# Kernel optimization log

Hardware: AMD Instinct MI355X
Metric: run time of the kernel (lower is better)

The kernel has to match this reference:

```python
import jax, jax.numpy as jnp
import numpy as np

NTOKEN = 150000   # len(ui2idx)
NINP   = 64       # opt.d_word_vec
NHID   = 2 * NINP # gnn1 output dim
NEDGE  = 2400000  # hetero static graph edges
B, L   = 64, 200  # batch_size, max_len


def setup_inputs() -> dict:
    key = jax.random.key(0)
    ks = jax.random.split(key, 8)
    def xavier(k, shape):
        scale = (2.0 / (shape[0] + shape[1])) ** 0.5
        return scale * jax.random.normal(k, shape, jnp.float32)
    emb = xavier(ks[0], (NTOKEN, NINP)).at[0].set(0.0)  # padding_idx=0
    W1 = xavier(ks[1], (NINP, NHID))
    b1 = jnp.zeros((NHID,), jnp.float32)
    W2 = xavier(ks[2], (NHID, NINP))
    b2 = jnp.zeros((NINP,), jnp.float32)
    edge_index = jax.random.randint(ks[3], (2, NEDGE), 0, NTOKEN, dtype=jnp.int32).astype(jnp.int64)
    inp = jax.random.randint(ks[4], (B, L), 0, NTOKEN, dtype=jnp.int32).astype(jnp.int64)
    input_timestamp = jax.random.randint(ks[5], (B, L), 0, 300000, dtype=jnp.int32).astype(jnp.int64)
    return {"emb": emb, "W1": W1, "b1": b1, "W2": W2, "b2": b2,
            "input": inp, "input_timestamp": input_timestamp, "edge_index": edge_index}


def gcn_conv(x, W, b, src, dst, n):
    # torch_geometric GCNConv: out = D^{-1/2}(A+I)D^{-1/2} (x W) + b
    h = x @ W                                   # [n, out]
    deg = jnp.zeros((n,), h.dtype).at[dst].add(1.0) + 1.0  # +1 self-loop
    dinv = jax.lax.rsqrt(deg)
    norm = dinv[src] * dinv[dst]                # [E]
    agg = jax.ops.segment_sum(h[src] * norm[:, None], dst, num_segments=n)
    return agg + h * (dinv * dinv)[:, None] + b  # self-loop term + bias


def reference(emb, W1, b1, W2, b2, input, input_timestamp, edge_index):
    src, dst = edge_index[0], edge_index[1]
    h = gcn_conv(emb, W1, b1, src, dst, NTOKEN)      # dropout is identity in eval
    nodes = gcn_conv(h, W2, b2, src, dst, NTOKEN)    # [NTOKEN, NINP]
    # one-hot scatter + einsum 'bt,td->bd' == direct gather
    b_, l_ = input.shape
    return nodes[input.reshape(-1)].reshape(b_, l_, NINP)
```

## Files before the change

kernel.cpp:

```cpp
#include <hip/hip_runtime.h>
#include <hip/hip_bf16.h>

#define NTOKEN 150000
#define NINP   64
#define NEDGE  2400000
#define NPOS   (64*200)

#define NPB    256
#define NBUCK  586
#define EPB    4096
#define NBLK   586
#define CAPS   4480

#define NXB    1172

#define O_XBF      0
#define O_Z1       4800000
#define O_BUCK     9600000
#define O_GCUR     12225280
#define O_DINV     12225920
#define O_RS       12375936
#define O_M        12525952
#define O_CVEC     12530048

__device__ __forceinline__ unsigned f2bf(float f) {
    unsigned u = __float_as_uint(f);
    return (u + 0x7FFFu + ((u >> 16) & 1u)) >> 16;
}

__global__ void __launch_bounds__(1024) k1(
        const float4* __restrict__ X4, uint4* __restrict__ Xbf,
        const float* __restrict__ W1, const float* __restrict__ b1,
        const float* __restrict__ W2, float* __restrict__ M,
        float* __restrict__ cvec, int* __restrict__ gcur) {
    int t = threadIdx.x, B = blockIdx.x;
    if (B < NXB) {
        int i = B * 1024 + t;
        if (i < NTOKEN * 64 / 8) {
            float4 a = X4[2 * i], b = X4[2 * i + 1];
            uint4 o;
            o.x = f2bf(a.x) | (f2bf(a.y) << 16);
            o.y = f2bf(a.z) | (f2bf(a.w) << 16);
            o.z = f2bf(b.x) | (f2bf(b.y) << 16);
            o.w = f2bf(b.z) | (f2bf(b.w) << 16);
            Xbf[i] = o;
        }
    } else if (B < NXB + 4) {
        int o = (B - NXB) * 1024 + t;
        int i = o >> 6, j = o & 63;
        float s = 0.f;
        #pragma unroll 4
        for (int k = 0; k < 128; k++) s = fmaf(W1[i * 128 + k], W2[k * 64 + j], s);
        M[o] = s;
    } else if (B == NXB + 4) {
        if (t < 64) {
            float s = 0.f;
            #pragma unroll 4
            for (int k = 0; k < 128; k++) s = fmaf(b1[k], W2[k * 64 + t], s);
            cvec[t] = s;
        }
    } else {
        if (t < NBUCK) gcur[t] = t * CAPS;
    }
}

__global__ void __launch_bounds__(512) kC(
        const int4* __restrict__ src4, const int4* __restrict__ dst4,
        int* __restrict__ gcur, int* __restrict__ bucketPacked) {
    __shared__ int eS[EPB];
    __shared__ int eD[EPB];
    __shared__ int h[NBUCK];
    int t = threadIdx.x, B = blockIdx.x;
    for (int i = t; i < NBUCK; i += 512) h[i] = 0;
    __syncthreads();
    int base4 = B * (EPB / 4);
    int n4 = NEDGE / 4 - base4; if (n4 > EPB / 4) n4 = EPB / 4;
    for (int i = t; i < n4; i += 512) {
        int4 s = src4[base4 + i];
        int4 d = dst4[base4 + i];
        eS[4*i+0] = s.x; eS[4*i+1] = s.y; eS[4*i+2] = s.z; eS[4*i+3] = s.w;
        eD[4*i+0] = d.x; eD[4*i+1] = d.y; eD[4*i+2] = d.z; eD[4*i+3] = d.w;
        atomicAdd(&h[d.x >> 8], 1);
        atomicAdd(&h[d.y >> 8], 1);
        atomicAdd(&h[d.z >> 8], 1);
        atomicAdd(&h[d.w >> 8], 1);
    }
    __syncthreads();
    for (int b = t; b < NBUCK; b += 512) {
        int c = h[b];
        if (c) h[b] = atomicAdd(&gcur[b], c);
    }
    __syncthreads();
    int n = n4 * 4;
    for (int i = t; i < n; i += 512) {
        int d = eD[i];
        int b = d >> 8;
        int pos = atomicAdd(&h[b], 1);
        bucketPacked[pos] = (eS[i] << 8) | (d & 255);
    }
}

__global__ void __launch_bounds__(512) kDS(
        const int* __restrict__ gcur,
        int* __restrict__ bucketPacked ,
        float* __restrict__ dinv, int* __restrict__ rowStart) {
    __shared__ int srt[CAPS];
    __shared__ int cnt[NPB];
    __shared__ int sd[NPB];
    int t = threadIdx.x, b = blockIdx.x;
    int e0 = b * CAPS;
    int nE = gcur[b] - e0;
    if (t < NPB) cnt[t] = 0;
    __syncthreads();
    for (int i = t; i < nE; i += 512) atomicAdd(&cnt[bucketPacked[e0 + i] & 255], 1);
    __syncthreads();
    int c = 0;
    if (t < NPB) { c = cnt[t]; sd[t] = c; }
    __syncthreads();
    for (int off = 1; off < 256; off <<= 1) {
        int x = 0;
        if (t < NPB && t >= off) x = sd[t - off];
        __syncthreads();
        if (t < NPB) sd[t] += x;
        __syncthreads();
    }
    if (t < NPB) {
        int excl = sd[t] - c;
        cnt[t] = excl;
        int node = b * NPB + t;
        if (node < NTOKEN) {
            dinv[node] = rsqrtf((float)c + 1.0f);
            rowStart[node] = (e0 + excl) | (c << 22);
        }
    }
    __syncthreads();
    for (int i = t; i < nE; i += 512) {
        int p = bucketPacked[e0 + i];
        int pos = atomicAdd(&cnt[p & 255], 1);
        srt[pos] = p >> 8;
    }
    __syncthreads();
    for (int i = t; i < nE; i += 512) bucketPacked[e0 + i] = srt[i];
}

__global__ void k_agg(const uint2* __restrict__ Xb, const float* __restrict__ dinv,
                      const int* __restrict__ rowStart, const int* __restrict__ sortedSrc,
                      uint2* __restrict__ Z1b) {
    int g = threadIdx.x >> 4;
    int fl = threadIdx.x & 15;
    int v = blockIdx.x * 16 + g;
    unsigned rs = (unsigned)rowStart[v];
    int e0 = rs & 0x3FFFFF;
    int e1 = e0 + (rs >> 22);
    float dv = dinv[v];
    uint2 xsw = Xb[(size_t)v * 16 + fl];
    float a0x=0.f,a0y=0.f,a0z=0.f,a0w=0.f, a1x=0.f,a1y=0.f,a1z=0.f,a1w=0.f;
    float a2x=0.f,a2y=0.f,a2z=0.f,a2w=0.f, a3x=0.f,a3y=0.f,a3z=0.f,a3w=0.f;
    for (int e = e0; e < e1; e += 8) {
        int m1=e+1<e1, m2=e+2<e1, m3=e+3<e1, m4=e+4<e1, m5=e+5<e1, m6=e+6<e1, m7=e+7<e1;
        int u0 = sortedSrc[e];
        int u1 = sortedSrc[m1 ? e+1 : e];
        int u2 = sortedSrc[m2 ? e+2 : e];
        int u3 = sortedSrc[m3 ? e+3 : e];
        int u4 = sortedSrc[m4 ? e+4 : e];
        int u5 = sortedSrc[m5 ? e+5 : e];
        int u6 = sortedSrc[m6 ? e+6 : e];
        int u7 = sortedSrc[m7 ? e+7 : e];
        float d0 = dinv[u0];
        float d1 = m1 ? dinv[u1] : 0.f;
        float d2 = m2 ? dinv[u2] : 0.f;
        float d3 = m3 ? dinv[u3] : 0.f;
        float d4 = m4 ? dinv[u4] : 0.f;
        float d5 = m5 ? dinv[u5] : 0.f;
        float d6 = m6 ? dinv[u6] : 0.f;
        float d7 = m7 ? dinv[u7] : 0.f;
        uint2 w0 = Xb[(size_t)u0 * 16 + fl];
        uint2 w1 = Xb[(size_t)u1 * 16 + fl];
        uint2 w2 = Xb[(size_t)u2 * 16 + fl];
        uint2 w3 = Xb[(size_t)u3 * 16 + fl];
        uint2 w4 = Xb[(size_t)u4 * 16 + fl];
        uint2 w5 = Xb[(size_t)u5 * 16 + fl];
        uint2 w6 = Xb[(size_t)u6 * 16 + fl];
        uint2 w7 = Xb[(size_t)u7 * 16 + fl];
        #define ACC(d,w,AX,AY,AZ,AW) \
            AX = fmaf(d, __uint_as_float((w).x << 16), AX); \
            AY = fmaf(d, __uint_as_float((w).x & 0xFFFF0000u), AY); \
            AZ = fmaf(d, __uint_as_float((w).y << 16), AZ); \
            AW = fmaf(d, __uint_as_float((w).y & 0xFFFF0000u), AW);
        ACC(d0,w0,a0x,a0y,a0z,a0w)
        ACC(d1,w1,a1x,a1y,a1z,a1w)
        ACC(d2,w2,a2x,a2y,a2z,a2w)
        ACC(d3,w3,a3x,a3y,a3z,a3w)
        ACC(d4,w4,a0x,a0y,a0z,a0w)
        ACC(d5,w5,a1x,a1y,a1z,a1w)
        ACC(d6,w6,a2x,a2y,a2z,a2w)
        ACC(d7,w7,a3x,a3y,a3z,a3w)
        #undef ACC
    }
    float ax = (a0x + a1x) + (a2x + a3x);
    float ay = (a0y + a1y) + (a2y + a3y);
    float az = (a0z + a1z) + (a2z + a3z);
    float aw = (a0w + a1w) + (a2w + a3w);
    float c = dv * dv;
    float ox = c * fmaf(dv, __uint_as_float(xsw.x << 16),         ax);
    float oy = c * fmaf(dv, __uint_as_float(xsw.x & 0xFFFF0000u), ay);
    float oz = c * fmaf(dv, __uint_as_float(xsw.y << 16),         az);
    float ow = c * fmaf(dv, __uint_as_float(xsw.y & 0xFFFF0000u), aw);
    uint2 o;
    o.x = f2bf(ox) | (f2bf(oy) << 16);
    o.y = f2bf(oz) | (f2bf(ow) << 16);
    Z1b[(size_t)v * 16 + fl] = o;
}

__global__ void k_out(const int* __restrict__ inp, const uint2* __restrict__ Z1b,
                      const float* __restrict__ dinv, const int* __restrict__ rowStart,
                      const int* __restrict__ sortedSrc, const float* __restrict__ M,
                      const float* __restrict__ cvec, const float* __restrict__ b2,
                      float* __restrict__ out) {
    int wid = threadIdx.x >> 6;
    int lane = threadIdx.x & 63;
    int g = lane >> 4, fl = lane & 15;
    int p = blockIdx.x * 4 + wid;
    if (p >= NPOS) return;
    int v = inp[p];
    unsigned rs = (unsigned)rowStart[v];
    int e0 = rs & 0x3FFFFF;
    int e1 = e0 + (rs >> 22);
    float ax0=0.f,ay0=0.f,az0=0.f,aw0=0.f,ss0=0.f;
    float ax1=0.f,ay1=0.f,az1=0.f,aw1=0.f,ss1=0.f;
    int e = e0 + g;
    for (; e + 4 < e1; e += 8) {
        int u0 = sortedSrc[e];
        int u1 = sortedSrc[e + 4];
        ss0 += dinv[u0]; ss1 += dinv[u1];
        uint2 z0 = Z1b[(size_t)u0 * 16 + fl];
        uint2 z1 = Z1b[(size_t)u1 * 16 + fl];
        ax0 += __uint_as_float(z0.x << 16);
        ay0 += __uint_as_float(z0.x & 0xFFFF0000u);
        az0 += __uint_as_float(z0.y << 16);
        aw0 += __uint_as_float(z0.y & 0xFFFF0000u);
        ax1 += __uint_as_float(z1.x << 16);
        ay1 += __uint_as_float(z1.x & 0xFFFF0000u);
        az1 += __uint_as_float(z1.y << 16);
        aw1 += __uint_as_float(z1.y & 0xFFFF0000u);
    }
    if (e < e1) {
        int u = sortedSrc[e];
        ss0 += dinv[u];
        uint2 z = Z1b[(size_t)u * 16 + fl];
        ax0 += __uint_as_float(z.x << 16);
        ay0 += __uint_as_float(z.x & 0xFFFF0000u);
        az0 += __uint_as_float(z.y << 16);
        aw0 += __uint_as_float(z.y & 0xFFFF0000u);
    }
    float ax = ax0 + ax1, ay = ay0 + ay1, az = az0 + az1, aw = aw0 + aw1, ss = ss0 + ss1;
    ax += __shfl_xor(ax, 16, 64); ay += __shfl_xor(ay, 16, 64);
    az += __shfl_xor(az, 16, 64); aw += __shfl_xor(aw, 16, 64);
    ss += __shfl_xor(ss, 16, 64);
    ax += __shfl_xor(ax, 32, 64); ay += __shfl_xor(ay, 32, 64);
    az += __shfl_xor(az, 32, 64); aw += __shfl_xor(aw, 32, 64);
    ss += __shfl_xor(ss, 32, 64);
    float dv = dinv[v];
    uint2 zs = Z1b[(size_t)v * 16 + fl];
    float z2x = dv * (ax + __uint_as_float(zs.x << 16));
    float z2y = dv * (ay + __uint_as_float(zs.x & 0xFFFF0000u));
    float z2z = dv * (az + __uint_as_float(zs.y << 16));
    float z2w = dv * (aw + __uint_as_float(zs.y & 0xFFFF0000u));
    float s = dv * (ss + dv);
    float o = fmaf(s, cvec[lane], b2[lane]);
    #pragma unroll
    for (int kb = 0; kb < 16; kb++) {
        float a0 = __shfl(z2x, kb, 64);
        float a1 = __shfl(z2y, kb, 64);
        float a2 = __shfl(z2z, kb, 64);
        float a3 = __shfl(z2w, kb, 64);
        o = fmaf(a0, M[(kb * 4 + 0) * 64 + lane], o);
        o = fmaf(a1, M[(kb * 4 + 1) * 64 + lane], o);
        o = fmaf(a2, M[(kb * 4 + 2) * 64 + lane], o);
        o = fmaf(a3, M[(kb * 4 + 3) * 64 + lane], o);
    }
    out[(size_t)p * 64 + lane] = o;
}

extern "C" void kernel_launch(void* const* d_in, const int* in_sizes, int n_in,
                              void* d_out, int out_size, void* d_ws, size_t ws_size,
                              hipStream_t stream) {
    const float* emb = (const float*)d_in[0];
    const float* W1  = (const float*)d_in[1];
    const float* b1  = (const float*)d_in[2];
    const float* W2  = (const float*)d_in[3];
    const float* b2  = (const float*)d_in[4];
    const int*   inp = (const int*)d_in[5];
    const int*   ei  = (const int*)d_in[7];
    const int* srcArr = ei;
    const int* dstArr = ei + NEDGE;
    float* out = (float*)d_out;

    float* ws         = (float*)d_ws;
    uint2* Xbf        = (uint2*)(ws + O_XBF);
    uint2* Z1b        = (uint2*)(ws + O_Z1);
    int*   buckPacked = (int*)ws + O_BUCK;
    int*   gcur       = (int*)ws + O_GCUR;
    float* dinv       = ws + O_DINV;
    int*   rowStart   = (int*)ws + O_RS;
    float* M          = ws + O_M;
    float* cvec       = ws + O_CVEC;

    k1    <<<NXB + 6, 1024, 0, stream>>>((const float4*)emb, (uint4*)Xbf,
                                         W1, b1, W2, M, cvec, gcur);
    kC    <<<NBLK, 512, 0, stream>>>((const int4*)srcArr, (const int4*)dstArr,
                                     gcur, buckPacked);
    kDS   <<<NBUCK, 512, 0, stream>>>(gcur, buckPacked, dinv, rowStart);
    k_agg <<<NTOKEN/16, 256, 0, stream>>>(Xbf, dinv, rowStart, buckPacked, Z1b);
    k_out <<<NPOS/4, 256, 0, stream>>>(inp, Z1b, dinv, rowStart,
                                       buckPacked, M, cvec, b2, out);
}
```

Before: 127.9 us.

## Fuse bf16 conversion and weight precompute into edge bucketing kernel

```diff
diff --git a/kernel.cpp b/kernel.cpp
--- a/kernel.cpp
+++ b/kernel.cpp
@@ -12,7 +12,7 @@
 #define NBLK   586
 #define CAPS   4480
 
-#define NXB    1172
+#define NCVT   2344
 
 #define O_XBF      0
 #define O_Z1       4800000
@@ -28,14 +28,47 @@
     return (u + 0x7FFFu + ((u >> 16) & 1u)) >> 16;
 }
 
-__global__ void __launch_bounds__(1024) k1(
+__global__ void __launch_bounds__(512) kCX(
+        const int4* __restrict__ src4, const int4* __restrict__ dst4,
+        int* __restrict__ gcur, int* __restrict__ bucketPacked,
         const float4* __restrict__ X4, uint4* __restrict__ Xbf,
         const float* __restrict__ W1, const float* __restrict__ b1,
         const float* __restrict__ W2, float* __restrict__ M,
-        float* __restrict__ cvec, int* __restrict__ gcur) {
+        float* __restrict__ cvec) {
+    __shared__ int eS[EPB];
+    __shared__ int eD[EPB];
+    __shared__ int h[NBUCK];
     int t = threadIdx.x, B = blockIdx.x;
-    if (B < NXB) {
-        int i = B * 1024 + t;
+    if (B < NBLK) {
+        for (int i = t; i < NBUCK; i += 512) h[i] = 0;
+        __syncthreads();
+        int base4 = B * (EPB / 4);
+        int n4 = NEDGE / 4 - base4; if (n4 > EPB / 4) n4 = EPB / 4;
+        for (int i = t; i < n4; i += 512) {
+            int4 s = src4[base4 + i];
+            int4 d = dst4[base4 + i];
+            eS[4*i+0] = s.x; eS[4*i+1] = s.y; eS[4*i+2] = s.z; eS[4*i+3] = s.w;
+            eD[4*i+0] = d.x; eD[4*i+1] = d.y; eD[4*i+2] = d.z; eD[4*i+3] = d.w;
+            atomicAdd(&h[d.x >> 8], 1);
+            atomicAdd(&h[d.y >> 8], 1);
+            atomicAdd(&h[d.z >> 8], 1);
+            atomicAdd(&h[d.w >> 8], 1);
+        }
+        __syncthreads();
+        for (int b = t; b < NBUCK; b += 512) {
+            int c = h[b];
+            if (c) h[b] = b * CAPS + atomicAdd(&gcur[b], c);
+        }
+        __syncthreads();
+        int n = n4 * 4;
+        for (int i = t; i < n; i += 512) {
+            int d = eD[i];
+            int b = d >> 8;
+            int pos = atomicAdd(&h[b], 1);
+            bucketPacked[pos] = (eS[i] << 8) | (d & 255);
+        }
+    } else if (B < NBLK + NCVT) {
+        int i = (B - NBLK) * 512 + t;
         if (i < NTOKEN * 64 / 8) {
             float4 a = X4[2 * i], b = X4[2 * i + 1];
             uint4 o;
@@ -45,58 +78,18 @@
             o.w = f2bf(b.z) | (f2bf(b.w) << 16);
             Xbf[i] = o;
         }
-    } else if (B < NXB + 4) {
-        int o = (B - NXB) * 1024 + t;
+    } else if (B < NBLK + NCVT + 8) {
+        int o = (B - NBLK - NCVT) * 512 + t;
         int i = o >> 6, j = o & 63;
         float s = 0.f;
         #pragma unroll 4
         for (int k = 0; k < 128; k++) s = fmaf(W1[i * 128 + k], W2[k * 64 + j], s);
         M[o] = s;
-    } else if (B == NXB + 4) {
-        if (t < 64) {
-            float s = 0.f;
-            #pragma unroll 4
-            for (int k = 0; k < 128; k++) s = fmaf(b1[k], W2[k * 64 + t], s);
-            cvec[t] = s;
-        }
-    } else {
-        if (t < NBUCK) gcur[t] = t * CAPS;
-    }
-}
-
-__global__ void __launch_bounds__(512) kC(
-        const int4* __restrict__ src4, const int4* __restrict__ dst4,
-        int* __restrict__ gcur, int* __restrict__ bucketPacked) {
-    __shared__ int eS[EPB];
-    __shared__ int eD[EPB];
-    __shared__ int h[NBUCK];
-    int t = threadIdx.x, B = blockIdx.x;
-    for (int i = t; i < NBUCK; i += 512) h[i] = 0;
-    __syncthreads();
-    int base4 = B * (EPB / 4);
-    int n4 = NEDGE / 4 - base4; if (n4 > EPB / 4) n4 = EPB / 4;
-    for (int i = t; i < n4; i += 512) {
-        int4 s = src4[base4 + i];
-        int4 d = dst4[base4 + i];
-        eS[4*i+0] = s.x; eS[4*i+1] = s.y; eS[4*i+2] = s.z; eS[4*i+3] = s.w;
-        eD[4*i+0] = d.x; eD[4*i+1] = d.y; eD[4*i+2] = d.z; eD[4*i+3] = d.w;
-        atomicAdd(&h[d.x >> 8], 1);
-        atomicAdd(&h[d.y >> 8], 1);
-        atomicAdd(&h[d.z >> 8], 1);
-        atomicAdd(&h[d.w >> 8], 1);
-    }
-    __syncthreads();
-    for (int b = t; b < NBUCK; b += 512) {
-        int c = h[b];
-        if (c) h[b] = atomicAdd(&gcur[b], c);
-    }
-    __syncthreads();
-    int n = n4 * 4;
-    for (int i = t; i < n; i += 512) {
-        int d = eD[i];
-        int b = d >> 8;
-        int pos = atomicAdd(&h[b], 1);
-        bucketPacked[pos] = (eS[i] << 8) | (d & 255);
+    } else if (t < 64) {
+        float s = 0.f;
+        #pragma unroll 4
+        for (int k = 0; k < 128; k++) s = fmaf(b1[k], W2[k * 64 + t], s);
+        cvec[t] = s;
     }
 }
 
@@ -109,7 +102,7 @@
     __shared__ int sd[NPB];
     int t = threadIdx.x, b = blockIdx.x;
     int e0 = b * CAPS;
-    int nE = gcur[b] - e0;
+    int nE = gcur[b];
     if (t < NPB) cnt[t] = 0;
     __syncthreads();
     for (int i = t; i < nE; i += 512) atomicAdd(&cnt[bucketPacked[e0 + i] & 255], 1);
@@ -306,10 +299,11 @@
     float* M          = ws + O_M;
     float* cvec       = ws + O_CVEC;
 
-    k1    <<<NXB + 6, 1024, 0, stream>>>((const float4*)emb, (uint4*)Xbf,
-                                         W1, b1, W2, M, cvec, gcur);
-    kC    <<<NBLK, 512, 0, stream>>>((const int4*)srcArr, (const int4*)dstArr,
-                                     gcur, buckPacked);
+    hipMemsetAsync(gcur, 0, NBUCK * sizeof(int), stream);
+    kCX   <<<NBLK + NCVT + 9, 512, 0, stream>>>((const int4*)srcArr, (const int4*)dstArr,
+                                                gcur, buckPacked,
+                                                (const float4*)emb, (uint4*)Xbf,
+                                                W1, b1, W2, M, cvec);
     kDS   <<<NBUCK, 512, 0, stream>>>(gcur, buckPacked, dinv, rowStart);
     k_agg <<<NTOKEN/16, 256, 0, stream>>>(Xbf, dinv, rowStart, buckPacked, Z1b);
     k_out <<<NPOS/4, 256, 0, stream>>>(inp, Z1b, dinv, rowStart,
```

New measurement: 129.3 us (median of 2 runs). Within noise of the previous version (+1.1%).
